# Optimization experiments

Hardware: AMD Instinct MI355X
Metric: run time of the kernel (lower is better)

Reference implementation:

```python
import jax, jax.numpy as jnp
import numpy as np
import math

NH = 12  # num_attention_heads (multiple of 4 required by pattern dispatch)


def _forward(Input, hidden_states, attention_mask, Wq, bq, Wk, bk, Wv, bv, Wo, bo, L):
    b, n, _, H = Input.shape
    hd = H // NH
    G = NH // 4  # heads per criss-cross pattern
    # boolean-mask gather of valid (head, tail) entity pairs, row-major like torch
    bi, ri, ci = jnp.nonzero(attention_mask > 0, size=L)
    x = Input[bi, ri, ci]            # [L, H] keys/values source
    xq = hidden_states[bi, ri, ci]   # [L, H] query source
    q = (xq @ Wq + bq).reshape(L, NH, hd)
    k = (x @ Wk + bk).reshape(L, NH, hd)
    v = (x @ Wv + bv).reshape(L, NH, hd)
    ar = jnp.arange(n)
    # per-pattern criss-cross masks for query position (b, r, c), each [L, n]
    m0 = attention_mask[bi, ri, :] * (ar[None, :] != ci[:, None])  # row r, exclude self col c
    m1 = attention_mask[bi, :, ci] * (ar[None, :] != ri[:, None])  # col c, exclude self row r
    m2 = attention_mask[bi, :, ri]                                  # col r (no self exclusion)
    m3 = attention_mask[bi, ci, :]                                  # row c (no self exclusion)
    adds = jnp.stack([(1.0 - m) * -10000.0 for m in (m0, m1, m2, m3)], axis=1)  # [L, 4, n]
    # scatter per-pattern head groups into zero grid, then criss-cross gather
    k_gs, v_gs = [], []
    for p in range(4):
        sk = jnp.zeros((b, n, n, G, hd), k.dtype).at[bi, ri, ci].set(k[:, p::4])
        sv = jnp.zeros((b, n, n, G, hd), v.dtype).at[bi, ri, ci].set(v[:, p::4])
        if p == 0:
            gk, gv = sk[bi, ri], sv[bi, ri]          # element [l,k] = grid[b, r, k]
        elif p == 1:
            gk, gv = sk[bi, :, ci], sv[bi, :, ci]    # grid[b, k, c]
        elif p == 2:
            gk, gv = sk[bi, :, ri], sv[bi, :, ri]    # grid[b, k, r]
        else:
            gk, gv = sk[bi, ci], sv[bi, ci]          # grid[b, c, k]
        k_gs.append(gk)
        v_gs.append(gv)
    kg = jnp.stack(k_gs, axis=1)  # [L, 4, n, G, hd]
    vg = jnp.stack(v_gs, axis=1)
    # head h = 4*g + p (k[:, p::4] picks heads p, p+4, p+8)
    kg = kg.transpose(0, 3, 1, 2, 4).reshape(L, NH, n, hd)
    vg = vg.transpose(0, 3, 1, 2, 4).reshape(L, NH, n, hd)
    amask = jnp.broadcast_to(adds[:, None, :, :], (L, G, 4, n)).reshape(L, NH, n)
    # prepend self key/value; NOTE: original code uses additive bias +1.0 (ones) for the self slot
    kf = jnp.concatenate([k[:, :, None, :], kg], axis=2)   # [L, NH, n+1, hd]
    vf = jnp.concatenate([v[:, :, None, :], vg], axis=2)
    amask = jnp.concatenate([jnp.ones((L, NH, 1), amask.dtype), amask], axis=-1)
    scores = jnp.einsum('lhd,lhkd->lhk', q, kf) / math.sqrt(hd) + amask
    probs = jax.nn.softmax(scores, axis=-1)  # dropout is identity in eval
    ctx = jnp.einsum('lhk,lhkd->lhd', probs, vf).reshape(L, H)
    return ctx @ Wo + bo


def setup_inputs() -> dict:
    key = jax.random.key(0)
    ks = jax.random.split(key, 8)
    b, n, H = 2, 40, 768
    Input = jax.random.normal(ks[0], (b, n, n, H), jnp.float32)
    hidden_states = jax.random.normal(ks[1], (b, n, n, H), jnp.float32)
    # all valid entity pairs except self pairs -> deterministic L
    attention_mask = (jnp.ones((b, n, n)) - jnp.eye(n)[None]).astype(jnp.float32)
    L = int(b * n * (n - 1))  # 3120
    std = 0.02
    Wq = std * jax.random.normal(ks[2], (H, H), jnp.float32)
    Wk = std * jax.random.normal(ks[3], (H, H), jnp.float32)
    Wv = std * jax.random.normal(ks[4], (H, H), jnp.float32)
    Wo = std * jax.random.normal(ks[5], (H, H), jnp.float32)
    bq = jnp.zeros((H,), jnp.float32)
    bk = jnp.zeros((H,), jnp.float32)
    bv = jnp.zeros((H,), jnp.float32)
    bo = jnp.zeros((H,), jnp.float32)
    return {"Input": Input, "hidden_states": hidden_states, "attention_mask": attention_mask,
            "Wq": Wq, "bq": bq, "Wk": Wk, "bk": bk, "Wv": Wv, "bv": bv, "Wo": Wo, "bo": bo, "L": L}


def reference(Input, hidden_states, attention_mask, Wq, bq, Wk, bk, Wv, bv, Wo, bo, L):
    return _forward(Input, hidden_states, attention_mask, Wq, bq, Wk, bk, Wv, bv, Wo, bo, L)
```

## Files before the change

kernel.cpp:

```cpp
#include <hip/hip_runtime.h>
#include <hip/hip_bf16.h>
#include <math.h>

#define NHEADS 12

typedef __attribute__((ext_vector_type(4))) float f32x4;
typedef __attribute__((ext_vector_type(16))) float f32x16;
typedef __attribute__((ext_vector_type(8))) short bf16x8;

__device__ __forceinline__ unsigned short f2bf(float x) {
  __hip_bfloat16 h = __float2bfloat16(x);
  return *reinterpret_cast<unsigned short*>(&h);
}
__device__ __forceinline__ float bf2f(unsigned short u) {
  union { unsigned int i; float f; } c; c.i = ((unsigned int)u) << 16; return c.f;
}

__device__ __forceinline__ int xcd_swz(int orig, int nwg) {
  int q = nwg >> 3, r = nwg & 7;
  int xcd = orig & 7, idx = orig >> 3;
  return (xcd < r ? xcd * (q + 1) : r * (q + 1) + (xcd - r) * q) + idx;
}

__global__ __launch_bounds__(256) void prep(const float* __restrict__ mask, int total,
                                            int* __restrict__ pos2l, int* __restrict__ lidx,
                                            const float* __restrict__ bk, const float* __restrict__ bv,
                                            float* __restrict__ bkv,
                                            const float* __restrict__ W0, const float* __restrict__ W1,
                                            const float* __restrict__ W2, const float* __restrict__ W3,
                                            unsigned short* __restrict__ T0, unsigned short* __restrict__ T1,
                                            unsigned short* __restrict__ T2, unsigned short* __restrict__ T3,
                                            int H) {
  int nt32 = H / 32;
  int nw = nt32 * nt32 * 4;
  int bx = blockIdx.x;
  int t = threadIdx.x;
  if (bx < nw) {
    __shared__ float tile[32][33];
    int z = bx / (nt32 * nt32);
    int rem = bx - z * nt32 * nt32;
    int byy = rem / nt32;
    int bxx = rem - byy * nt32;
    const float* W = (z == 0) ? W0 : (z == 1) ? W1 : (z == 2) ? W2 : W3;
    unsigned short* T = (z == 0) ? T0 : (z == 1) ? T1 : (z == 2) ? T2 : T3;
    int k0 = byy * 32, n0 = bxx * 32;
    int kk = t >> 3, n4 = (t & 7) * 4;
    float4 v = *reinterpret_cast<const float4*>(W + (size_t)(k0 + kk) * H + n0 + n4);
    tile[n4 + 0][kk] = v.x; tile[n4 + 1][kk] = v.y; tile[n4 + 2][kk] = v.z; tile[n4 + 3][kk] = v.w;
    __syncthreads();
    int nn2 = t >> 3, k4 = (t & 7) * 4;
#pragma unroll
    for (int e = 0; e < 4; ++e)
      T[(size_t)(n0 + nn2) * H + k0 + k4 + e] = f2bf(tile[nn2][k4 + e]);
  } else {
    __shared__ int cnt[256];
    for (int i = t; i < H; i += 256) { bkv[i] = bk[i]; bkv[H + i] = bv[i]; }
    int per = (total + 255) >> 8;
    int begin = t * per;
    int end = begin + per; if (end > total) end = total;
    if (begin > total) begin = total;
    int c = 0;
    for (int i = begin; i < end; ++i) c += (mask[i] > 0.f) ? 1 : 0;
    cnt[t] = c;
    __syncthreads();
    for (int off = 1; off < 256; off <<= 1) {
      int vv = (t >= off) ? cnt[t - off] : 0;
      __syncthreads();
      cnt[t] += vv;
      __syncthreads();
    }
    int excl = cnt[t] - c;
    for (int i = begin; i < end; ++i) {
      if (mask[i] > 0.f) { pos2l[i] = excl; lidx[excl] = i; ++excl; }
      else pos2l[i] = -1;
    }
  }
}

#define QBM 128
#define QBN 128
#define QBK 64

__device__ __forceinline__ void gemm128_f32a_core(const float* __restrict__ A,
                                                  const int* __restrict__ lidx,
                                                  const unsigned short* __restrict__ Bt,
                                                  const float* __restrict__ bias,
                                                  unsigned short* __restrict__ C,
                                                  int M, int N, int K, int m0, int n0,
                                                  unsigned short* sA, unsigned short* sB) {
  int tid = threadIdx.x;
  int wid = tid >> 6, lane = tid & 63;
  int wm = wid >> 1, wn = wid & 1;
  int lane31 = lane & 31, laneh = lane >> 5;
  f32x16 acc[2][2] = {};

  const float* aptr[4];
  const unsigned short* bptr[4];
  int ldsoff[4];
#pragma unroll
  for (int r = 0; r < 4; ++r) {
    int c = (r * 4 + wid) * 64 + lane;
    int row = c >> 3, sl = c & 7;
    int sg = sl ^ (row & 7);
    int gm = m0 + row; if (gm >= M) gm = M - 1;
    aptr[r] = A + (size_t)lidx[gm] * K + sg * 8;
    bptr[r] = Bt + (size_t)(n0 + row) * K + sg * 8;
    ldsoff[r] = c * 8;
  }

  for (int k0 = 0; k0 < K; k0 += QBK) {
#pragma unroll
    for (int r = 0; r < 4; ++r)
      __builtin_amdgcn_global_load_lds((const __attribute__((address_space(1))) unsigned int*)(bptr[r] + k0),
                                       (__attribute__((address_space(3))) unsigned int*)(sB + (r * 4 + wid) * 512),
                                       16, 0, 0);
    bf16x8 st[4];
#pragma unroll
    for (int r = 0; r < 4; ++r) {
      f32x4 a = *reinterpret_cast<const f32x4*>(aptr[r] + k0);
      f32x4 b = *reinterpret_cast<const f32x4*>(aptr[r] + k0 + 4);
#pragma unroll
      for (int e = 0; e < 4; ++e) { st[r][e] = f2bf(a[e]); st[r][4 + e] = f2bf(b[e]); }
    }
#pragma unroll
    for (int r = 0; r < 4; ++r)
      *reinterpret_cast<bf16x8*>(sA + ldsoff[r]) = st[r];
    __syncthreads();
#pragma unroll
    for (int ks = 0; ks < 4; ++ks) {
      bf16x8 af[2], bfr[2];
#pragma unroll
      for (int i = 0; i < 2; ++i) {
        int row = wm * 64 + i * 32 + lane31;
        int slot = (ks * 2 + laneh) ^ (row & 7);
        af[i] = *reinterpret_cast<const bf16x8*>(sA + row * 64 + slot * 8);
      }
#pragma unroll
      for (int j = 0; j < 2; ++j) {
        int rn = wn * 64 + j * 32 + lane31;
        int slot = (ks * 2 + laneh) ^ (rn & 7);
        bfr[j] = *reinterpret_cast<const bf16x8*>(sB + rn * 64 + slot * 8);
      }
#pragma unroll
      for (int i = 0; i < 2; ++i)
#pragma unroll
        for (int j = 0; j < 2; ++j)
          acc[i][j] = __builtin_amdgcn_mfma_f32_32x32x16_bf16(af[i], bfr[j], acc[i][j], 0, 0, 0);
    }
    __syncthreads();
  }

#pragma unroll
  for (int i = 0; i < 2; ++i) {
#pragma unroll
    for (int j = 0; j < 2; ++j) {
      int gcol = n0 + wn * 64 + j * 32 + lane31;
      float bv = bias[gcol];
#pragma unroll
      for (int r = 0; r < 16; ++r) {
        int gm = m0 + wm * 64 + i * 32 + (r & 3) + ((r >> 2) << 3) + (laneh << 2);
        if (gm >= M) continue;
        C[(size_t)gm * N + gcol] = f2bf(acc[i][j][r] + bv);
      }
    }
  }
}

__global__ __launch_bounds__(256) void gemm_qkv(const float* __restrict__ hidden,
                                                const float* __restrict__ input,
                                                const unsigned short* __restrict__ Wqt,
                                                const unsigned short* __restrict__ Wkvt,
                                                const float* __restrict__ bq,
                                                const float* __restrict__ bkv,
                                                const int* __restrict__ lidx,
                                                unsigned short* __restrict__ Cq,
                                                unsigned short* __restrict__ Ckv,
                                                int M, int K, int H, int NX) {
  __shared__ unsigned short sA[QBM * QBK];
  __shared__ unsigned short sB[QBN * QBK];
  int wgid = xcd_swz(blockIdx.x, gridDim.x);
  int y = wgid / NX, x = wgid - y * NX;
  int m0 = y * QBM;
  int nq = H / QBN;
  if (x < nq)
    gemm128_f32a_core(hidden, lidx, Wqt, bq, Cq, M, H, K, m0, x * QBN, sA, sB);
  else
    gemm128_f32a_core(input, lidx, Wkvt, bkv, Ckv, M, 2 * H, K, m0, (x - nq) * QBN, sA, sB);
}

#define GBM 128
#define GBN 64
#define GBK 64

__global__ __launch_bounds__(256) void gemm_out(const unsigned short* __restrict__ A,
                                                const unsigned short* __restrict__ Bt,
                                                const float* __restrict__ bias,
                                                float* __restrict__ C,
                                                int M, int N, int K) {
  __shared__ unsigned short sA[GBM * GBK];
  __shared__ unsigned short sB[GBN * GBK];
  int NX = N / GBN;
  int wgid = xcd_swz(blockIdx.x, gridDim.x);
  int y = wgid / NX, x = wgid - y * NX;
  int m0 = y * GBM, n0 = x * GBN;
  int tid = threadIdx.x;
  int wid = tid >> 6, lane = tid & 63;
  int wm = wid >> 1, wn = wid & 1;
  int lane31 = lane & 31, laneh = lane >> 5;
  f32x16 acc[2] = {};

  const unsigned short* aptr[4];
  const unsigned short* bptr[2];
#pragma unroll
  for (int r = 0; r < 4; ++r) {
    int c = (r * 4 + wid) * 64 + lane;
    int row = c >> 3, sl = c & 7;
    int sg = sl ^ (row & 7);
    aptr[r] = A + (size_t)(m0 + row) * K + sg * 8;
    if (r < 2) bptr[r] = Bt + (size_t)(n0 + row) * K + sg * 8;
  }

  for (int k0 = 0; k0 < K; k0 += GBK) {
#pragma unroll
    for (int r = 0; r < 4; ++r)
      __builtin_amdgcn_global_load_lds((const __attribute__((address_space(1))) unsigned int*)(aptr[r] + k0),
                                       (__attribute__((address_space(3))) unsigned int*)(sA + (r * 4 + wid) * 512),
                                       16, 0, 0);
#pragma unroll
    for (int r = 0; r < 2; ++r)
      __builtin_amdgcn_global_load_lds((const __attribute__((address_space(1))) unsigned int*)(bptr[r] + k0),
                                       (__attribute__((address_space(3))) unsigned int*)(sB + (r * 4 + wid) * 512),
                                       16, 0, 0);
    __syncthreads();
#pragma unroll
    for (int ks = 0; ks < 4; ++ks) {
      bf16x8 af[2], bfr;
#pragma unroll
      for (int i = 0; i < 2; ++i) {
        int row = wm * 64 + i * 32 + lane31;
        int slot = (ks * 2 + laneh) ^ (row & 7);
        af[i] = *reinterpret_cast<const bf16x8*>(sA + row * 64 + slot * 8);
      }
      {
        int rn = wn * 32 + lane31;
        int slot = (ks * 2 + laneh) ^ (rn & 7);
        bfr = *reinterpret_cast<const bf16x8*>(sB + rn * 64 + slot * 8);
      }
#pragma unroll
      for (int i = 0; i < 2; ++i)
        acc[i] = __builtin_amdgcn_mfma_f32_32x32x16_bf16(af[i], bfr, acc[i], 0, 0, 0);
    }
    __syncthreads();
  }

#pragma unroll
  for (int i = 0; i < 2; ++i) {
    int gcol = n0 + wn * 32 + lane31;
    float bv = bias[gcol];
#pragma unroll
    for (int r = 0; r < 16; ++r) {
      int gm = m0 + wm * 64 + i * 32 + (r & 3) + ((r >> 2) << 3) + (laneh << 2);
      if (gm >= M) continue;
      C[(size_t)gm * N + gcol] = acc[i][r] + bv;
    }
  }
}

__global__ __launch_bounds__(128) void attn3(const unsigned short* __restrict__ qb,
                                             const unsigned short* __restrict__ KVb,
                                             const float* __restrict__ mask,
                                             const int* __restrict__ pos2l,
                                             unsigned short* __restrict__ ctx,
                                             int n, int H) {
  __shared__ unsigned short Ks[40 * 72];
  __shared__ unsigned short Vs[40 * 72];
  __shared__ float S[40][44];
  __shared__ float Sinv[40];
  __shared__ float mrow[40];
  __shared__ int qlist[40];

  int bx = blockIdx.x;
  int r0 = bx % n;
  int h3 = (bx / n) % 3;
  int p = (bx / (3 * n)) % 4;
  int bi = bx / (12 * n);
  int h = p + 4 * h3;
  int nn = n * n;
  bool rowkeys = (p == 0 || p == 3);
  bool rowq = (p == 0 || p == 2);
  bool excl = (p < 2);
  int t = threadIdx.x;
  int H2 = 2 * H;

#pragma unroll
  for (int i = 0; i < 5; ++i) {
    int c2 = t + 128 * i;
    int jr = c2 >> 3, e8 = c2 & 7;
    int half = jr >= 40 ? 1 : 0;
    int j = jr - half * 40;
    int keypos = rowkeys ? (r0 * n + j) : (j * n + r0);
    int l2 = pos2l[bi * nn + keypos];
    bf16x8 v = {};
    if (l2 >= 0)
      v = *reinterpret_cast<const bf16x8*>(KVb + (size_t)l2 * H2 + half * H + h * 64 + e8 * 8);
    *reinterpret_cast<bf16x8*>((half ? Vs : Ks) + j * 72 + e8 * 8) = v;
  }
  if (t < 40) {
    mrow[t] = rowkeys ? mask[bi * nn + r0 * n + t] : mask[bi * nn + t * n + r0];
    int qpos = rowq ? (r0 * n + t) : (t * n + r0);
    qlist[t] = pos2l[bi * nn + qpos];
  }
  __syncthreads();

  int c = t % 40;
  int role = t / 40;
  int lq = (t < 120) ? qlist[c] : -1;

  if (lq >= 0) {
    float qf[64];
    const unsigned short* qp = qb + (size_t)lq * H + h * 64;
#pragma unroll
    for (int e8 = 0; e8 < 8; ++e8) {
      bf16x8 t8 = *reinterpret_cast<const bf16x8*>(qp + e8 * 8);
#pragma unroll
      for (int e = 0; e < 8; ++e) qf[e8 * 8 + e] = bf2f((unsigned short)t8[e]);
    }
    int j0 = role * 14;
    int j1 = j0 + 14; if (j1 > 40) j1 = 40;
    for (int j = j0; j < j1; ++j) {
      float acc = 0.f;
#pragma unroll
      for (int e8 = 0; e8 < 8; ++e8) {
        bf16x8 kv = *reinterpret_cast<const bf16x8*>(Ks + j * 72 + e8 * 8);
#pragma unroll
        for (int e = 0; e < 8; ++e) acc = fmaf(qf[e8 * 8 + e], bf2f((unsigned short)kv[e]), acc);
      }
      float mval = mrow[j] * ((excl && j == c) ? 0.f : 1.f);
      S[c][j] = acc * 0.125f + (1.f - mval) * -10000.f;
    }
    if (role == 2) {
      const unsigned short* kp = KVb + (size_t)lq * H2 + h * 64;
      float acc = 0.f;
#pragma unroll
      for (int e8 = 0; e8 < 8; ++e8) {
        bf16x8 kv = *reinterpret_cast<const bf16x8*>(kp + e8 * 8);
#pragma unroll
        for (int e = 0; e < 8; ++e) acc = fmaf(qf[e8 * 8 + e], bf2f((unsigned short)kv[e]), acc);
      }
      S[c][40] = acc * 0.125f + 1.0f;
    }
  }
  __syncthreads();

  if (t < 40 && qlist[t] >= 0) {
    float mx = S[t][0];
    for (int j = 1; j <= 40; ++j) mx = fmaxf(mx, S[t][j]);
    float sum = 0.f;
    for (int j = 0; j <= 40; ++j) { float e = __expf(S[t][j] - mx); S[t][j] = e; sum += e; }
    Sinv[t] = 1.f / sum;
  }
  __syncthreads();

  if (t < 80 && lq >= 0) {
    int d0 = role * 32;
    const unsigned short* vsp = KVb + (size_t)lq * H2 + H + h * 64 + d0;
    float pself = S[c][40];
    float inv = Sinv[c];
#pragma unroll
    for (int ch = 0; ch < 4; ++ch) {
      int dd = d0 + ch * 8;
      float facc[8];
      bf16x8 vself = *reinterpret_cast<const bf16x8*>(vsp + ch * 8);
#pragma unroll
      for (int e = 0; e < 8; ++e) facc[e] = pself * bf2f((unsigned short)vself[e]);
      for (int j = 0; j < 40; ++j) {
        float pj = S[c][j];
        bf16x8 vv = *reinterpret_cast<const bf16x8*>(Vs + j * 72 + dd);
#pragma unroll
        for (int e = 0; e < 8; ++e) facc[e] = fmaf(pj, bf2f((unsigned short)vv[e]), facc[e]);
      }
      bf16x8 st;
#pragma unroll
      for (int e = 0; e < 8; ++e) st[e] = f2bf(facc[e] * inv);
      *reinterpret_cast<bf16x8*>(ctx + (size_t)lq * H + h * 64 + dd) = st;
    }
  }
}

extern "C" void kernel_launch(void* const* d_in, const int* in_sizes, int n_in,
                              void* d_out, int out_size, void* d_ws, size_t ws_size,
                              hipStream_t stream) {
  const float* Input  = (const float*)d_in[0];
  const float* hidden = (const float*)d_in[1];
  const float* mask   = (const float*)d_in[2];
  const float* Wq = (const float*)d_in[3];
  const float* bq = (const float*)d_in[4];
  const float* Wk = (const float*)d_in[5];
  const float* bk = (const float*)d_in[6];
  const float* Wv = (const float*)d_in[7];
  const float* bv = (const float*)d_in[8];
  const float* Wo = (const float*)d_in[9];
  const float* bo = (const float*)d_in[10];

  int H = (int)llround(sqrt((double)in_sizes[3]));
  int total = in_sizes[2];
  int L = out_size / H;
  int bn = total - L;
  int n = total / bn;
  int b = bn / n;
  int mtiles = (L + QBM - 1) / QBM;
  int Mpad = mtiles * QBM;
  size_t aElems = (size_t)Mpad * H;

  char* p = (char*)d_ws;
  auto take = [&](size_t bytes) { char* r = p; p += (bytes + 255) & ~(size_t)255; return r; };
  int* lidx  = (int*)take((size_t)L * 4);
  int* pos2l = (int*)take((size_t)total * 4);
  float* bkv = (float*)take((size_t)2 * H * 4);
  unsigned short* Wqt  = (unsigned short*)take((size_t)H * H * 2);
  unsigned short* Wot  = (unsigned short*)take((size_t)H * H * 2);
  unsigned short* Wkvt = (unsigned short*)take((size_t)2 * H * H * 2);
  unsigned short* qb2  = (unsigned short*)take(aElems * 2);
  unsigned short* KVb  = (unsigned short*)take(aElems * 2 * 2);
  unsigned short* ctxb = (unsigned short*)take(aElems * 2);

  int nt32 = H / 32;
  int nwconv = nt32 * nt32 * 4;
  prep<<<nwconv + 1, 256, 0, stream>>>(mask, total, pos2l, lidx, bk, bv, bkv,
                                       Wq, Wk, Wv, Wo,
                                       Wqt, Wkvt, Wkvt + (size_t)H * H, Wot, H);
  {
    int NX = 3 * H / QBN;
    gemm_qkv<<<NX * mtiles, 256, 0, stream>>>(hidden, Input, Wqt, Wkvt, bq, bkv, lidx,
                                              qb2, KVb, L, H, H, NX);
  }
  attn3<<<b * 4 * 3 * n, 128, 0, stream>>>(qb2, KVb, mask, pos2l, ctxb, n, H);
  gemm_out<<<(H / GBN) * mtiles, 256, 0, stream>>>(ctxb, Wot, bo, (float*)d_out, L, H, H);
}
```

Measured before the change: 84.15 us.

## Double-buffer LDS tiles in QKV and output GEMMs to overlap loads with MFMA

Both GEMM kernels now use two LDS buffers per operand. The next K-tile is prefetched (async global_load_lds for bf16 operands, register loads plus bf16 conversion for the fp32 A operand) while MFMAs run on the current tile, and the trailing barrier per iteration is removed. The goal is to hide global memory latency behind compute. The cost is doubled LDS use per block, which may lower occupancy, and more live registers for the prefetched fp32 A data.

```diff
diff --git a/kernel.cpp b/kernel.cpp
--- a/kernel.cpp
+++ b/kernel.cpp
@@ -108,24 +108,46 @@
     ldsoff[r] = c * 8;
   }
 
-  for (int k0 = 0; k0 < K; k0 += QBK) {
-#pragma unroll
-    for (int r = 0; r < 4; ++r)
-      __builtin_amdgcn_global_load_lds((const __attribute__((address_space(1))) unsigned int*)(bptr[r] + k0),
-                                       (__attribute__((address_space(3))) unsigned int*)(sB + (r * 4 + wid) * 512),
-                                       16, 0, 0);
+  const int nt = K / QBK;
+#pragma unroll
+  for (int r = 0; r < 4; ++r)
+    __builtin_amdgcn_global_load_lds((const __attribute__((address_space(1))) unsigned int*)bptr[r],
+                                     (__attribute__((address_space(3))) unsigned int*)(sB + (r * 4 + wid) * 512),
+                                     16, 0, 0);
+  {
     bf16x8 st[4];
 #pragma unroll
     for (int r = 0; r < 4; ++r) {
-      f32x4 a = *reinterpret_cast<const f32x4*>(aptr[r] + k0);
-      f32x4 b = *reinterpret_cast<const f32x4*>(aptr[r] + k0 + 4);
+      f32x4 a = *reinterpret_cast<const f32x4*>(aptr[r]);
+      f32x4 b = *reinterpret_cast<const f32x4*>(aptr[r] + 4);
 #pragma unroll
       for (int e = 0; e < 4; ++e) { st[r][e] = f2bf(a[e]); st[r][4 + e] = f2bf(b[e]); }
     }
 #pragma unroll
     for (int r = 0; r < 4; ++r)
       *reinterpret_cast<bf16x8*>(sA + ldsoff[r]) = st[r];
+  }
+
+  int cur = 0;
+  for (int t = 0; t < nt; ++t) {
     __syncthreads();
+    int k1 = (t + 1) * QBK;
+    bool more = (t + 1 < nt);
+    f32x4 an[4], bn[4];
+    if (more) {
+#pragma unroll
+      for (int r = 0; r < 4; ++r) {
+        an[r] = *reinterpret_cast<const f32x4*>(aptr[r] + k1);
+        bn[r] = *reinterpret_cast<const f32x4*>(aptr[r] + k1 + 4);
+      }
+#pragma unroll
+      for (int r = 0; r < 4; ++r)
+        __builtin_amdgcn_global_load_lds((const __attribute__((address_space(1))) unsigned int*)(bptr[r] + k1),
+                                         (__attribute__((address_space(3))) unsigned int*)(sB + (cur ^ 1) * (QBN * QBK) + (r * 4 + wid) * 512),
+                                         16, 0, 0);
+    }
+    const unsigned short* pA = sA + cur * (QBM * QBK);
+    const unsigned short* pB = sB + cur * (QBN * QBK);
 #pragma unroll
     for (int ks = 0; ks < 4; ++ks) {
       bf16x8 af[2], bfr[2];
@@ -133,13 +155,13 @@
       for (int i = 0; i < 2; ++i) {
         int row = wm * 64 + i * 32 + lane31;
         int slot = (ks * 2 + laneh) ^ (row & 7);
-        af[i] = *reinterpret_cast<const bf16x8*>(sA + row * 64 + slot * 8);
+        af[i] = *reinterpret_cast<const bf16x8*>(pA + row * 64 + slot * 8);
       }
 #pragma unroll
       for (int j = 0; j < 2; ++j) {
         int rn = wn * 64 + j * 32 + lane31;
         int slot = (ks * 2 + laneh) ^ (rn & 7);
-        bfr[j] = *reinterpret_cast<const bf16x8*>(sB + rn * 64 + slot * 8);
+        bfr[j] = *reinterpret_cast<const bf16x8*>(pB + rn * 64 + slot * 8);
       }
 #pragma unroll
       for (int i = 0; i < 2; ++i)
@@ -147,7 +169,18 @@
         for (int j = 0; j < 2; ++j)
           acc[i][j] = __builtin_amdgcn_mfma_f32_32x32x16_bf16(af[i], bfr[j], acc[i][j], 0, 0, 0);
     }
-    __syncthreads();
+    if (more) {
+      bf16x8 st[4];
+#pragma unroll
+      for (int r = 0; r < 4; ++r) {
+#pragma unroll
+        for (int e = 0; e < 4; ++e) { st[r][e] = f2bf(an[r][e]); st[r][4 + e] = f2bf(bn[r][e]); }
+      }
+#pragma unroll
+      for (int r = 0; r < 4; ++r)
+        *reinterpret_cast<bf16x8*>(sA + (cur ^ 1) * (QBM * QBK) + ldsoff[r]) = st[r];
+    }
+    cur ^= 1;
   }
 
 #pragma unroll
@@ -176,8 +209,8 @@
                                                 unsigned short* __restrict__ Cq,
                                                 unsigned short* __restrict__ Ckv,
                                                 int M, int K, int H, int NX) {
-  __shared__ unsigned short sA[QBM * QBK];
-  __shared__ unsigned short sB[QBN * QBK];
+  __shared__ unsigned short sA[2 * QBM * QBK];
+  __shared__ unsigned short sB[2 * QBN * QBK];
   int wgid = xcd_swz(blockIdx.x, gridDim.x);
   int y = wgid / NX, x = wgid - y * NX;
   int m0 = y * QBM;
@@ -197,8 +230,8 @@
                                                 const float* __restrict__ bias,
                                                 float* __restrict__ C,
                                                 int M, int N, int K) {
-  __shared__ unsigned short sA[GBM * GBK];
-  __shared__ unsigned short sB[GBN * GBK];
+  __shared__ unsigned short sA[2 * GBM * GBK];
+  __shared__ unsigned short sB[2 * GBN * GBK];
   int NX = N / GBN;
   int wgid = xcd_swz(blockIdx.x, gridDim.x);
   int y = wgid / NX, x = wgid - y * NX;
@@ -220,18 +253,27 @@
     if (r < 2) bptr[r] = Bt + (size_t)(n0 + row) * K + sg * 8;
   }
 
-  for (int k0 = 0; k0 < K; k0 += GBK) {
+  auto STAGE = [&](int buf, int k0) {
 #pragma unroll
     for (int r = 0; r < 4; ++r)
       __builtin_amdgcn_global_load_lds((const __attribute__((address_space(1))) unsigned int*)(aptr[r] + k0),
-                                       (__attribute__((address_space(3))) unsigned int*)(sA + (r * 4 + wid) * 512),
+                                       (__attribute__((address_space(3))) unsigned int*)(sA + buf * (GBM * GBK) + (r * 4 + wid) * 512),
                                        16, 0, 0);
 #pragma unroll
     for (int r = 0; r < 2; ++r)
       __builtin_amdgcn_global_load_lds((const __attribute__((address_space(1))) unsigned int*)(bptr[r] + k0),
-                                       (__attribute__((address_space(3))) unsigned int*)(sB + (r * 4 + wid) * 512),
+                                       (__attribute__((address_space(3))) unsigned int*)(sB + buf * (GBN * GBK) + (r * 4 + wid) * 512),
                                        16, 0, 0);
+  };
+
+  const int nt = K / GBK;
+  STAGE(0, 0);
+  int cur = 0;
+  for (int t = 0; t < nt; ++t) {
     __syncthreads();
+    if (t + 1 < nt) STAGE(cur ^ 1, (t + 1) * GBK);
+    const unsigned short* pA = sA + cur * (GBM * GBK);
+    const unsigned short* pB = sB + cur * (GBN * GBK);
 #pragma unroll
     for (int ks = 0; ks < 4; ++ks) {
       bf16x8 af[2], bfr;
@@ -239,18 +281,18 @@
       for (int i = 0; i < 2; ++i) {
         int row = wm * 64 + i * 32 + lane31;
         int slot = (ks * 2 + laneh) ^ (row & 7);
-        af[i] = *reinterpret_cast<const bf16x8*>(sA + row * 64 + slot * 8);
+        af[i] = *reinterpret_cast<const bf16x8*>(pA + row * 64 + slot * 8);
       }
       {
         int rn = wn * 32 + lane31;
         int slot = (ks * 2 + laneh) ^ (rn & 7);
-        bfr = *reinterpret_cast<const bf16x8*>(sB + rn * 64 + slot * 8);
+        bfr = *reinterpret_cast<const bf16x8*>(pB + rn * 64 + slot * 8);
       }
 #pragma unroll
       for (int i = 0; i < 2; ++i)
         acc[i] = __builtin_amdgcn_mfma_f32_32x32x16_bf16(af[i], bfr, acc[i], 0, 0, 0);
     }
-    __syncthreads();
+    cur ^= 1;
   }
 
 #pragma unroll
```

Result: no change. 85.23 us (+1.3%).
